# Kernel tuning notes

Hardware: AMD Instinct MI355X
Metric: run time of the kernel (lower is better)

## Reference

```python
import jax, jax.numpy as jnp
import numpy as np

NV = 100000   # vehicle nodes
NE = 100000   # 'edge' nodes (dst type)
E = 250000    # graph edges (connects relation)
VDIM = 16
EDIM = 16
HID = 128
HEADS = 4
DH = 128      # out_feats per head (GATv2Conv(hid, hid))
EPS = 1e-5
NEG_SLOPE = 0.2


def _layernorm(x, g, b):
    mu = x.mean(-1, keepdims=True)
    var = ((x - mu) ** 2).mean(-1, keepdims=True)
    return (x - mu) * jax.lax.rsqrt(var + EPS) * g + b


def setup_inputs() -> dict:
    key = jax.random.key(0)
    ks = jax.random.split(key, 20)
    s = 0.05
    return {
        "v_feat": jax.random.normal(ks[0], (NV, VDIM), jnp.float32),
        "e_feat": jax.random.normal(ks[1], (NE, EDIM), jnp.float32),
        "Wv": jax.random.normal(ks[2], (VDIM, HID), jnp.float32) * s,
        "bv": jnp.zeros((HID,), jnp.float32),
        "gv": jnp.ones((HID,), jnp.float32),
        "betav": jnp.zeros((HID,), jnp.float32),
        "We": jax.random.normal(ks[3], (EDIM, HID), jnp.float32) * s,
        "be": jnp.zeros((HID,), jnp.float32),
        "ge": jnp.ones((HID,), jnp.float32),
        "betae": jnp.zeros((HID,), jnp.float32),
        "Wsrc": jax.random.normal(ks[4], (HID, HEADS * DH), jnp.float32) * s,
        "bsrc": jnp.zeros((HEADS * DH,), jnp.float32),
        "Wdst": jax.random.normal(ks[5], (HID, HEADS * DH), jnp.float32) * s,
        "bdst": jnp.zeros((HEADS * DH,), jnp.float32),
        "attn": jax.random.normal(ks[6], (HEADS, DH), jnp.float32) * s,
        "Wp": jax.random.normal(ks[7], (HID, HID), jnp.float32) * s,
        "bp": jnp.zeros((HID,), jnp.float32),
        "src": jax.random.randint(ks[8], (E,), 0, NV, jnp.int32),
        "dst": jax.random.randint(ks[9], (E,), 0, NE, jnp.int32),
    }


def reference(v_feat, e_feat, Wv, bv, gv, betav, We, be, ge, betae,
              Wsrc, bsrc, Wdst, bdst, attn, Wp, bp, src, dst):
    # --- node-type encoders: Linear -> ReLU -> LayerNorm ---
    h_v = _layernorm(jax.nn.relu(v_feat @ Wv + bv), gv, betav)      # [NV, HID]
    h_e = _layernorm(jax.nn.relu(e_feat @ We + be), ge, betae)      # [NE, HID]

    # --- GATv2Conv (bipartite: vehicle -> edge), 4 heads ---
    fs = (h_v @ Wsrc + bsrc).reshape(NV, HEADS, DH)                 # src proj
    fd = (h_e @ Wdst + bdst).reshape(NE, HEADS, DH)                 # dst proj
    e = jax.nn.leaky_relu(fs[src] + fd[dst], NEG_SLOPE)             # [E, H, D]
    score = jnp.einsum("ehd,hd->eh", e, attn)                       # [E, H]
    # segment-wise (per-dst-node) softmax over incoming edges
    smax = jax.ops.segment_max(score, dst, num_segments=NE)         # [NE, H]
    ex = jnp.exp(score - smax[dst])
    denom = jax.ops.segment_sum(ex, dst, num_segments=NE)
    alpha = ex / denom[dst]                                         # [E, H]
    out = jax.ops.segment_sum(alpha[:, :, None] * fs[src], dst,
                              num_segments=NE)                      # [NE, H, D]

    # HeteroGraphConv mean-aggregate (single relation -> identity),
    # then mean over heads (edge_out.dim()==3 branch)
    edge_out = out.mean(axis=1)                                     # [NE, HID]

    # feature_proj: Linear -> ReLU -> Dropout(eval: identity)
    return jax.nn.relu(edge_out @ Wp + bp)
```

## Files before the change

kernel.cpp:

```cpp
#include <hip/hip_runtime.h>
#include <hip/hip_bf16.h>
#include <math.h>

#define NV 100000
#define NE_N 100000
#define NEDGE 250000
#define NPAD 100032
#define NEG 0.2f
#define LN_EPS 1e-5f

typedef __bf16 bf16_t;
typedef __bf16 bf16x8 __attribute__((ext_vector_type(8)));
typedef float f32x4 __attribute__((ext_vector_type(4)));

__device__ inline unsigned short f2bfu(float f) {
    return __builtin_bit_cast(unsigned short, (__bf16)f);
}
__device__ inline float bfu2f(unsigned short u) {
    return (float)__builtin_bit_cast(__bf16, u);
}
__device__ inline float blo(unsigned w) { return __uint_as_float(w << 16); }
__device__ inline float bhi(unsigned w) { return __uint_as_float(w & 0xffff0000u); }
__device__ inline float lrelu(float x) { return x > 0.f ? x : NEG * x; }
__device__ inline unsigned pk2(float a, float b) {
    return (unsigned)f2bfu(a) | ((unsigned)f2bfu(b) << 16);
}

__device__ __forceinline__ void gload_lds16(const void* g, void* l) {
    __builtin_amdgcn_global_load_lds(
        (const __attribute__((address_space(1))) unsigned int*)g,
        (__attribute__((address_space(3))) unsigned int*)l,
        16, 0, 0);
}

__global__ __launch_bounds__(256) void prep_kernel(
    const float* __restrict__ Wsrc, const float* __restrict__ Wdst,
    const float* __restrict__ Wp, bf16_t* __restrict__ pS,
    bf16_t* __restrict__ pD, bf16_t* __restrict__ pP)
{
    int t = blockIdx.x * 256 + threadIdx.x;
    if (t < 8192) {
        int ksq = t >> 9, col = t & 511;
#pragma unroll
        for (int j = 0; j < 8; ++j)
            pS[(size_t)t * 8 + j] = (bf16_t)Wsrc[(ksq * 8 + j) * 512 + col];
    } else if (t < 16384) {
        int g = t - 8192;
        int ksq = g >> 9, col = g & 511;
#pragma unroll
        for (int j = 0; j < 8; ++j)
            pD[(size_t)g * 8 + j] = (bf16_t)Wdst[(ksq * 8 + j) * 512 + col];
    } else if (t < 18432) {
        int g = t - 16384;
        int ksq = g >> 7, col = g & 127;
#pragma unroll
        for (int j = 0; j < 8; ++j)
            pP[(size_t)g * 8 + j] = (bf16_t)Wp[(ksq * 8 + j) * 128 + col];
    }
}

__global__ __launch_bounds__(256) void count_kernel(
    const int* __restrict__ dst, int* __restrict__ deg)
{
    int t = blockIdx.x * 256 + threadIdx.x;
    if (t < NEDGE) atomicAdd(&deg[dst[t]], 1);
}

__global__ __launch_bounds__(256) void scan1_kernel(
    const int* __restrict__ deg, int* __restrict__ offs, int* __restrict__ bsum)
{
    __shared__ int s[256];
    int i = blockIdx.x * 256 + threadIdx.x;
    int v = (i < NE_N) ? deg[i] : 0;
    s[threadIdx.x] = v;
    __syncthreads();
    for (int off = 1; off < 256; off <<= 1) {
        int t_ = (threadIdx.x >= off) ? s[threadIdx.x - off] : 0;
        __syncthreads();
        s[threadIdx.x] += t_;
        __syncthreads();
    }
    if (i < NE_N) offs[i] = s[threadIdx.x] - v;
    if (threadIdx.x == 255) bsum[blockIdx.x] = s[255];
}

__global__ __launch_bounds__(512) void scan2_kernel(int* __restrict__ bsum, int nb)
{
    __shared__ int s[512];
    int t = threadIdx.x;
    int v = (t < nb) ? bsum[t] : 0;
    s[t] = v;
    __syncthreads();
    for (int off = 1; off < 512; off <<= 1) {
        int t_ = (t >= off) ? s[t - off] : 0;
        __syncthreads();
        s[t] += t_;
        __syncthreads();
    }
    if (t < nb) bsum[t] = s[t] - v;
}

__global__ __launch_bounds__(256) void scan3_kernel(
    int* __restrict__ offs, const int* __restrict__ bsum, int* __restrict__ cursor)
{
    int i = blockIdx.x * 256 + threadIdx.x;
    if (i < NE_N) {
        int o = offs[i] + bsum[blockIdx.x];
        offs[i] = o;
        cursor[i] = o;
    }
}

__global__ __launch_bounds__(256) void scatter_kernel(
    const int* __restrict__ dst, int* __restrict__ cursor, int* __restrict__ eidx)
{
    int t = blockIdx.x * 256 + threadIdx.x;
    if (t < NEDGE) {
        int pos = atomicAdd(&cursor[dst[t]], 1);
        eidx[pos] = t;
    }
}

__global__ __launch_bounds__(256, 4) void enc_proj_kernel(
    const float* __restrict__ featV, const float* __restrict__ WencV,
    const float* __restrict__ bencV, const float* __restrict__ gV,
    const float* __restrict__ betaV, const bf16_t* __restrict__ ApackV,
    const float* __restrict__ bprojV, unsigned short* __restrict__ outV,
    const float* __restrict__ featE, const float* __restrict__ WencE,
    const float* __restrict__ bencE, const float* __restrict__ gE,
    const float* __restrict__ betaE, const bf16_t* __restrict__ ApackE,
    const float* __restrict__ bprojE, unsigned short* __restrict__ outE,
    int nblk1, int M)
{
    __shared__ unsigned short Hs[64 * 136];
    __shared__ __align__(16) unsigned short Abuf[2][8192];
    __shared__ __align__(16) float Bias[512];

    int b = blockIdx.x;
    bool isV = b < nblk1;
    const float* feat  = isV ? featV  : featE;
    const float* Wenc  = isV ? WencV  : WencE;
    const float* benc  = isV ? bencV  : bencE;
    const float* gln   = isV ? gV     : gE;
    const float* beta  = isV ? betaV  : betaE;
    const bf16_t* Apack = isV ? ApackV : ApackE;
    const float* bproj = isV ? bprojV : bprojE;
    unsigned short* out = isV ? outV : outE;
    int row0 = (isV ? b : b - nblk1) * 64;

    int t = threadIdx.x;
    int l = t & 63;
    int w = t >> 6;
    int rbase = __builtin_amdgcn_readfirstlane(w * 16);

    {
        int sr = row0 + rbase + (l >> 2);
        if (sr > M - 1) sr = M - 1;
        gload_lds16(feat + (size_t)sr * 16 + (l & 3) * 4, &Abuf[1][w * 512]);
    }

#pragma unroll
    for (int j = 0; j < 4; ++j) {
        int ksq = w * 4 + j;
        gload_lds16(Apack + ((size_t)(ksq * 512) + l) * 8, &Abuf[0][ksq * 512]);
    }
    if (t < 128)
        *(float4*)&Bias[t * 4] = *(const float4*)(bproj + t * 4);

    float wc0[16], wc1[16];
#pragma unroll
    for (int k = 0; k < 16; ++k) {
        float2 wv = *(const float2*)(Wenc + k * 128 + 2 * l);
        wc0[k] = wv.x;
        wc1[k] = wv.y;
    }
    float2 bv2 = *(const float2*)(benc + 2 * l);

    asm volatile("s_waitcnt vmcnt(0)" ::: "memory");

    const float* Fs = (const float*)&Abuf[1][0];
#pragma unroll
    for (int i = 0; i < 16; ++i) {
        const float* fr = Fs + (rbase + i) * 16;
        float4 f0 = *(const float4*)(fr);
        float4 f1 = *(const float4*)(fr + 4);
        float4 f2 = *(const float4*)(fr + 8);
        float4 f3 = *(const float4*)(fr + 12);
        float a0 = bv2.x, a1 = bv2.y;
        a0 = fmaf(f0.x, wc0[0], a0);  a1 = fmaf(f0.x, wc1[0], a1);
        a0 = fmaf(f0.y, wc0[1], a0);  a1 = fmaf(f0.y, wc1[1], a1);
        a0 = fmaf(f0.z, wc0[2], a0);  a1 = fmaf(f0.z, wc1[2], a1);
        a0 = fmaf(f0.w, wc0[3], a0);  a1 = fmaf(f0.w, wc1[3], a1);
        a0 = fmaf(f1.x, wc0[4], a0);  a1 = fmaf(f1.x, wc1[4], a1);
        a0 = fmaf(f1.y, wc0[5], a0);  a1 = fmaf(f1.y, wc1[5], a1);
        a0 = fmaf(f1.z, wc0[6], a0);  a1 = fmaf(f1.z, wc1[6], a1);
        a0 = fmaf(f1.w, wc0[7], a0);  a1 = fmaf(f1.w, wc1[7], a1);
        a0 = fmaf(f2.x, wc0[8], a0);  a1 = fmaf(f2.x, wc1[8], a1);
        a0 = fmaf(f2.y, wc0[9], a0);  a1 = fmaf(f2.y, wc1[9], a1);
        a0 = fmaf(f2.z, wc0[10], a0); a1 = fmaf(f2.z, wc1[10], a1);
        a0 = fmaf(f2.w, wc0[11], a0); a1 = fmaf(f2.w, wc1[11], a1);
        a0 = fmaf(f3.x, wc0[12], a0); a1 = fmaf(f3.x, wc1[12], a1);
        a0 = fmaf(f3.y, wc0[13], a0); a1 = fmaf(f3.y, wc1[13], a1);
        a0 = fmaf(f3.z, wc0[14], a0); a1 = fmaf(f3.z, wc1[14], a1);
        a0 = fmaf(f3.w, wc0[15], a0); a1 = fmaf(f3.w, wc1[15], a1);
        a0 = fmaxf(a0, 0.f);
        a1 = fmaxf(a1, 0.f);
        *(unsigned*)&Hs[(rbase + i) * 136 + 2 * l] = pk2(a0, a1);
    }

    float s = 0.f, s2 = 0.f;
    {
        int rr = rbase + (l >> 2);
        int q = l & 3;
#pragma unroll
        for (int j = 0; j < 4; ++j) {
            uint4 v = *(const uint4*)&Hs[rr * 136 + q * 32 + j * 8];
            float x;
            x = blo(v.x); s += x; s2 = fmaf(x, x, s2);
            x = bhi(v.x); s += x; s2 = fmaf(x, x, s2);
            x = blo(v.y); s += x; s2 = fmaf(x, x, s2);
            x = bhi(v.y); s += x; s2 = fmaf(x, x, s2);
            x = blo(v.z); s += x; s2 = fmaf(x, x, s2);
            x = bhi(v.z); s += x; s2 = fmaf(x, x, s2);
            x = blo(v.w); s += x; s2 = fmaf(x, x, s2);
            x = bhi(v.w); s += x; s2 = fmaf(x, x, s2);
        }
    }
    s  += __shfl_xor(s, 1, 64);  s  += __shfl_xor(s, 2, 64);
    s2 += __shfl_xor(s2, 1, 64); s2 += __shfl_xor(s2, 2, 64);
    float mu  = s * (1.f / 128.f);
    float var = s2 * (1.f / 128.f) - mu * mu;
    float inv = rsqrtf(var + LN_EPS);

    int kq = l >> 4;
    int ln = l & 15;
    float mu_r  = __shfl(mu,  ln * 4, 64);
    float inv_r = __shfl(inv, ln * 4, 64);

    bf16x8 bfr[4];
#pragma unroll
    for (int ks = 0; ks < 4; ++ks) {
        int c0 = ks * 32 + kq * 8;
        uint4 v = *(const uint4*)&Hs[(rbase + ln) * 136 + c0];
        float4 g0 = *(const float4*)(gln + c0);
        float4 g1 = *(const float4*)(gln + c0 + 4);
        float4 b0 = *(const float4*)(beta + c0);
        float4 b1 = *(const float4*)(beta + c0 + 4);
        uint4 p;
        p.x = pk2(fmaf((blo(v.x) - mu_r) * inv_r, g0.x, b0.x),
                  fmaf((bhi(v.x) - mu_r) * inv_r, g0.y, b0.y));
        p.y = pk2(fmaf((blo(v.y) - mu_r) * inv_r, g0.z, b0.z),
                  fmaf((bhi(v.y) - mu_r) * inv_r, g0.w, b0.w));
        p.z = pk2(fmaf((blo(v.z) - mu_r) * inv_r, g1.x, b1.x),
                  fmaf((bhi(v.z) - mu_r) * inv_r, g1.y, b1.y));
        p.w = pk2(fmaf((blo(v.w) - mu_r) * inv_r, g1.z, b1.z),
                  fmaf((bhi(v.w) - mu_r) * inv_r, g1.w, b1.w));
        bfr[ks] = __builtin_bit_cast(bf16x8, p);
    }

    unsigned short* stag = Hs + rbase * 136;
    int node = row0 + rbase + ln;

#pragma unroll
    for (int p = 0; p < 8; ++p) {
        if (p == 0)
            asm volatile("s_waitcnt lgkmcnt(0)" ::: "memory");
        else
            asm volatile("s_waitcnt vmcnt(2)" ::: "memory");
        __builtin_amdgcn_s_barrier();

        if (p < 7) {
#pragma unroll
            for (int j = 0; j < 4; ++j) {
                int ksq = w * 4 + j;
                gload_lds16(Apack + ((size_t)(ksq * 512 + (p + 1) * 64) + l) * 8,
                            &Abuf[(p + 1) & 1][ksq * 512]);
            }
            __builtin_amdgcn_sched_barrier(0);
        }

        const unsigned short* Ac = Abuf[p & 1];
#pragma unroll
        for (int mt = 0; mt < 4; ++mt) {
            bf16x8 a[4];
#pragma unroll
            for (int ks = 0; ks < 4; ++ks)
                a[ks] = *(const bf16x8*)&Ac[((ks * 4 + kq) * 64 + mt * 16 + ln) * 8];

            f32x4 acc = {0.f, 0.f, 0.f, 0.f};
#pragma unroll
            for (int ks = 0; ks < 4; ++ks)
                acc = __builtin_amdgcn_mfma_f32_16x16x32_bf16(a[ks], bfr[ks], acc, 0, 0, 0);

            int colp = p * 64 + mt * 16 + kq * 4;
            float4 bb = *(const float4*)&Bias[colp];
            ushort4 o;
            o.x = f2bfu(acc[0] + bb.x);
            o.y = f2bfu(acc[1] + bb.y);
            o.z = f2bfu(acc[2] + bb.z);
            o.w = f2bfu(acc[3] + bb.w);
            *(ushort4*)&stag[ln * 136 + mt * 16 + kq * 4] = o;
        }
#pragma unroll
        for (int i = 0; i < 2; ++i) {
            uint4 v = *(const uint4*)&stag[ln * 136 + i * 32 + kq * 8];
            *(uint4*)(out + (size_t)node * 512 + p * 64 + i * 32 + kq * 8) = v;
        }
    }
}

__global__ __launch_bounds__(256) void final_gemm_kernel(
    const float* __restrict__ A, const bf16_t* __restrict__ Ppack,
    const float* __restrict__ bp, float* __restrict__ C, int M)
{
    __shared__ unsigned short Hs[64 * 136];
    int t = threadIdx.x;
    int lane = t & 63;
    int w = t >> 6;
    int row0 = blockIdx.x * 64;

#pragma unroll
    for (int i = 0; i < 8; ++i) {
        int f4 = i * 256 + t;
        int r = f4 >> 5;
        int c4 = (f4 & 31) * 4;
        float4 v = make_float4(0.f, 0.f, 0.f, 0.f);
        if (row0 + r < M)
            v = ((const float4*)(A + (size_t)(row0 + r) * 128))[f4 & 31];
        ushort4 o;
        o.x = f2bfu(v.x); o.y = f2bfu(v.y); o.z = f2bfu(v.z); o.w = f2bfu(v.w);
        *(ushort4*)&Hs[r * 136 + c4] = o;
    }
    __syncthreads();

    int kq = lane >> 4;
    int ln = lane & 15;

    f32x4 acc[2][4];
#pragma unroll
    for (int mt = 0; mt < 2; ++mt)
#pragma unroll
        for (int nt = 0; nt < 4; ++nt) {
            f32x4 z = {0.f, 0.f, 0.f, 0.f};
            acc[mt][nt] = z;
        }

#pragma unroll
    for (int ks = 0; ks < 4; ++ks) {
        bf16x8 bfr[4];
#pragma unroll
        for (int nt = 0; nt < 4; ++nt) {
            const uint4* p = (const uint4*)&Hs[(nt * 16 + ln) * 136 + ks * 32 + kq * 8];
            bfr[nt] = __builtin_bit_cast(bf16x8, *p);
        }
        bf16x8 afr[2];
#pragma unroll
        for (int mt = 0; mt < 2; ++mt) {
            int colA = w * 32 + mt * 16 + ln;
            afr[mt] = *(const bf16x8*)(Ppack + ((size_t)(ks * 4 + kq) * 128 + colA) * 8);
        }
#pragma unroll
        for (int mt = 0; mt < 2; ++mt)
#pragma unroll
            for (int nt = 0; nt < 4; ++nt)
                acc[mt][nt] = __builtin_amdgcn_mfma_f32_16x16x32_bf16(
                    afr[mt], bfr[nt], acc[mt][nt], 0, 0, 0);
    }

#pragma unroll
    for (int mt = 0; mt < 2; ++mt) {
        int col = w * 32 + mt * 16 + kq * 4;
        float4 bb = *(const float4*)(bp + col);
#pragma unroll
        for (int nt = 0; nt < 4; ++nt) {
            int node = row0 + nt * 16 + ln;
            if (node < M) {
                float4 o;
                o.x = fmaxf(acc[mt][nt][0] + bb.x, 0.f);
                o.y = fmaxf(acc[mt][nt][1] + bb.y, 0.f);
                o.z = fmaxf(acc[mt][nt][2] + bb.z, 0.f);
                o.w = fmaxf(acc[mt][nt][3] + bb.w, 0.f);
                *(float4*)(C + (size_t)node * 128 + col) = o;
            }
        }
    }
}

__global__ __launch_bounds__(256) void softagg_kernel(
    const unsigned short* __restrict__ fs, const unsigned short* __restrict__ fdp,
    const float* __restrict__ attn, const int* __restrict__ src,
    const int* __restrict__ offs, const int* __restrict__ deg,
    const int* __restrict__ eidx, float* __restrict__ out)
{
    int d = blockIdx.x * 4 + (threadIdx.x >> 6);
    if (d >= NE_N) return;
    int l = threadIdx.x & 63;
    int r0 = offs[d];
    int n = deg[d];
    int o = l * 8;

    uint4 fv = *(const uint4*)(fdp + (size_t)d * 512 + o);
    float fdv[8] = { blo(fv.x), bhi(fv.x), blo(fv.y), bhi(fv.y),
                     blo(fv.z), bhi(fv.z), blo(fv.w), bhi(fv.w) };
    float4 w0 = *(const float4*)(attn + o);
    float4 w1 = *(const float4*)(attn + o + 4);
    float wv[8] = { w0.x, w0.y, w0.z, w0.w, w1.x, w1.y, w1.z, w1.w };

    float m = -1e30f, sm = 0.f;
    float acc[8];
#pragma unroll
    for (int j = 0; j < 8; ++j) acc[j] = 0.f;

    for (int base = 0; base < n; base += 64) {
        int cnt = min(n - base, 64);
        int sl = 0;
        if (l < cnt) sl = src[eidx[r0 + base + l]];
        for (int i = 0; i < cnt; ++i) {
            int s = __shfl(sl, i, 64);
            uint4 a = *(const uint4*)(fs + (size_t)s * 512 + o);
            float fsv[8] = { blo(a.x), bhi(a.x), blo(a.y), bhi(a.y),
                             blo(a.z), bhi(a.z), blo(a.w), bhi(a.w) };
            float p = 0.f;
#pragma unroll
            for (int j = 0; j < 8; ++j)
                p = fmaf(lrelu(fsv[j] + fdv[j]), wv[j], p);
#pragma unroll
            for (int mk = 1; mk < 16; mk <<= 1)
                p += __shfl_xor(p, mk, 64);
            float mn = fmaxf(m, p);
            float c  = __expf(m - mn);
            float av = __expf(p - mn);
            sm = sm * c + av;
            m = mn;
#pragma unroll
            for (int j = 0; j < 8; ++j)
                acc[j] = fmaf(av, fsv[j], acc[j] * c);
        }
    }

    float inv = (n > 0) ? 0.25f / sm : 0.f;
#pragma unroll
    for (int j = 0; j < 8; ++j) {
        float v = acc[j] * inv;
        v += __shfl_xor(v, 16, 64);
        v += __shfl_xor(v, 32, 64);
        acc[j] = v;
    }
    if (l < 16) {
        float4 o0 = make_float4(acc[0], acc[1], acc[2], acc[3]);
        float4 o1 = make_float4(acc[4], acc[5], acc[6], acc[7]);
        *(float4*)(out + (size_t)d * 128 + l * 8) = o0;
        *(float4*)(out + (size_t)d * 128 + l * 8 + 4) = o1;
    }
}

extern "C" void kernel_launch(void* const* d_in, const int* in_sizes, int n_in,
                              void* d_out, int out_size, void* d_ws, size_t ws_size,
                              hipStream_t stream)
{
    const float* v_feat = (const float*)d_in[0];
    const float* e_feat = (const float*)d_in[1];
    const float* Wv     = (const float*)d_in[2];
    const float* bv     = (const float*)d_in[3];
    const float* gv     = (const float*)d_in[4];
    const float* betav  = (const float*)d_in[5];
    const float* We     = (const float*)d_in[6];
    const float* be     = (const float*)d_in[7];
    const float* ge     = (const float*)d_in[8];
    const float* betae  = (const float*)d_in[9];
    const float* Wsrc   = (const float*)d_in[10];
    const float* bsrc   = (const float*)d_in[11];
    const float* Wdst   = (const float*)d_in[12];
    const float* bdst   = (const float*)d_in[13];
    const float* attn   = (const float*)d_in[14];
    const float* Wp     = (const float*)d_in[15];
    const float* bp     = (const float*)d_in[16];
    const int*   src    = (const int*)d_in[17];
    const int*   dst    = (const int*)d_in[18];
    float* out = (float*)d_out;

    unsigned short* fs = (unsigned short*)d_ws;
    unsigned short* fd = fs + (size_t)NPAD * 512;
    int* deg    = (int*)(fd + (size_t)NPAD * 512);
    int* offs   = deg + NE_N;
    int* cursor = offs + NE_N;
    int* bsum   = cursor + NE_N;
    int* eidx   = bsum + 512;
    bf16_t* pS  = (bf16_t*)(eidx + NEDGE);
    bf16_t* pD  = pS + 65536;
    bf16_t* pP  = pD + 65536;

    const int NB_SCAN = (NE_N + 255) / 256;

    prep_kernel<<<72, 256, 0, stream>>>(Wsrc, Wdst, Wp, pS, pD, pP);

    hipMemsetAsync(deg, 0, (size_t)NE_N * sizeof(int), stream);
    count_kernel<<<(NEDGE + 255) / 256, 256, 0, stream>>>(dst, deg);
    scan1_kernel<<<NB_SCAN, 256, 0, stream>>>(deg, offs, bsum);
    scan2_kernel<<<1, 512, 0, stream>>>(bsum, NB_SCAN);
    scan3_kernel<<<NB_SCAN, 256, 0, stream>>>(offs, bsum, cursor);
    scatter_kernel<<<(NEDGE + 255) / 256, 256, 0, stream>>>(dst, cursor, eidx);

    enc_proj_kernel<<<3126, 256, 0, stream>>>(
        v_feat, Wv, bv, gv, betav, pS, bsrc, fs,
        e_feat, We, be, ge, betae, pD, bdst, fd,
        1563, 100000);

    softagg_kernel<<<NE_N / 4, 256, 0, stream>>>(fs, fd, attn, src, offs, deg,
                                                 eidx, out);

    final_gemm_kernel<<<1563, 256, 0, stream>>>(out, pP, bp, out, NE_N);
}
```

Measured before the change: 297.7 us.

## Fold deg memset into prep, enlarge encoder blocks, pass bf16 intermediate to final GEMM

Zeroes the degree array inside prep_kernel so the separate memset launch is gone. The encoder/projection kernel now uses 512-thread blocks covering 128 rows, which halves the number of blocks and shares each packed-weight load across more rows. Its encoder FMAs are written as packed 2-wide float operations. The aggregation kernel writes its output as bf16 into a workspace buffer, and the final GEMM reads it directly, cutting intermediate traffic and the fp32-to-bf16 conversion. This relies on enough workspace for the extra buffer, the larger LDS footprint per block may reduce occupancy, and NPAD grows to cover the 128-row tiles.

```diff
diff --git a/kernel.cpp b/kernel.cpp
--- a/kernel.cpp
+++ b/kernel.cpp
@@ -5,19 +5,17 @@
 #define NV 100000
 #define NE_N 100000
 #define NEDGE 250000
-#define NPAD 100032
+#define NPAD 100096
 #define NEG 0.2f
 #define LN_EPS 1e-5f
 
 typedef __bf16 bf16_t;
 typedef __bf16 bf16x8 __attribute__((ext_vector_type(8)));
 typedef float f32x4 __attribute__((ext_vector_type(4)));
+typedef float f32x2 __attribute__((ext_vector_type(2)));
 
 __device__ inline unsigned short f2bfu(float f) {
     return __builtin_bit_cast(unsigned short, (__bf16)f);
-}
-__device__ inline float bfu2f(unsigned short u) {
-    return (float)__builtin_bit_cast(__bf16, u);
 }
 __device__ inline float blo(unsigned w) { return __uint_as_float(w << 16); }
 __device__ inline float bhi(unsigned w) { return __uint_as_float(w & 0xffff0000u); }
@@ -36,7 +34,8 @@
 __global__ __launch_bounds__(256) void prep_kernel(
     const float* __restrict__ Wsrc, const float* __restrict__ Wdst,
     const float* __restrict__ Wp, bf16_t* __restrict__ pS,
-    bf16_t* __restrict__ pD, bf16_t* __restrict__ pP)
+    bf16_t* __restrict__ pD, bf16_t* __restrict__ pP,
+    int* __restrict__ deg)
 {
     int t = blockIdx.x * 256 + threadIdx.x;
     if (t < 8192) {
@@ -56,6 +55,9 @@
 #pragma unroll
         for (int j = 0; j < 8; ++j)
             pP[(size_t)g * 8 + j] = (bf16_t)Wp[(ksq * 8 + j) * 128 + col];
+    } else {
+        int z = t - 18432;
+        if (z < NE_N) deg[z] = 0;
     }
 }
 
@@ -121,7 +123,7 @@
     }
 }
 
-__global__ __launch_bounds__(256, 4) void enc_proj_kernel(
+__global__ __launch_bounds__(512, 4) void enc_proj_kernel(
     const float* __restrict__ featV, const float* __restrict__ WencV,
     const float* __restrict__ bencV, const float* __restrict__ gV,
     const float* __restrict__ betaV, const bf16_t* __restrict__ ApackV,
@@ -132,7 +134,7 @@
     const float* __restrict__ bprojE, unsigned short* __restrict__ outE,
     int nblk1, int M)
 {
-    __shared__ unsigned short Hs[64 * 136];
+    __shared__ unsigned short Hs[128 * 136];
     __shared__ __align__(16) unsigned short Abuf[2][8192];
     __shared__ __align__(16) float Bias[512];
 
@@ -146,7 +148,7 @@
     const bf16_t* Apack = isV ? ApackV : ApackE;
     const float* bproj = isV ? bprojV : bprojE;
     unsigned short* out = isV ? outV : outE;
-    int row0 = (isV ? b : b - nblk1) * 64;
+    int row0 = (isV ? b : b - nblk1) * 128;
 
     int t = threadIdx.x;
     int l = t & 63;
@@ -160,19 +162,19 @@
     }
 
 #pragma unroll
-    for (int j = 0; j < 4; ++j) {
-        int ksq = w * 4 + j;
+    for (int j = 0; j < 2; ++j) {
+        int ksq = w * 2 + j;
         gload_lds16(Apack + ((size_t)(ksq * 512) + l) * 8, &Abuf[0][ksq * 512]);
     }
     if (t < 128)
         *(float4*)&Bias[t * 4] = *(const float4*)(bproj + t * 4);
 
-    float wc0[16], wc1[16];
+    f32x2 wc2[16];
 #pragma unroll
     for (int k = 0; k < 16; ++k) {
         float2 wv = *(const float2*)(Wenc + k * 128 + 2 * l);
-        wc0[k] = wv.x;
-        wc1[k] = wv.y;
+        wc2[k][0] = wv.x;
+        wc2[k][1] = wv.y;
     }
     float2 bv2 = *(const float2*)(benc + 2 * l);
 
@@ -186,25 +188,25 @@
         float4 f1 = *(const float4*)(fr + 4);
         float4 f2 = *(const float4*)(fr + 8);
         float4 f3 = *(const float4*)(fr + 12);
-        float a0 = bv2.x, a1 = bv2.y;
-        a0 = fmaf(f0.x, wc0[0], a0);  a1 = fmaf(f0.x, wc1[0], a1);
-        a0 = fmaf(f0.y, wc0[1], a0);  a1 = fmaf(f0.y, wc1[1], a1);
-        a0 = fmaf(f0.z, wc0[2], a0);  a1 = fmaf(f0.z, wc1[2], a1);
-        a0 = fmaf(f0.w, wc0[3], a0);  a1 = fmaf(f0.w, wc1[3], a1);
-        a0 = fmaf(f1.x, wc0[4], a0);  a1 = fmaf(f1.x, wc1[4], a1);
-        a0 = fmaf(f1.y, wc0[5], a0);  a1 = fmaf(f1.y, wc1[5], a1);
-        a0 = fmaf(f1.z, wc0[6], a0);  a1 = fmaf(f1.z, wc1[6], a1);
-        a0 = fmaf(f1.w, wc0[7], a0);  a1 = fmaf(f1.w, wc1[7], a1);
-        a0 = fmaf(f2.x, wc0[8], a0);  a1 = fmaf(f2.x, wc1[8], a1);
-        a0 = fmaf(f2.y, wc0[9], a0);  a1 = fmaf(f2.y, wc1[9], a1);
-        a0 = fmaf(f2.z, wc0[10], a0); a1 = fmaf(f2.z, wc1[10], a1);
-        a0 = fmaf(f2.w, wc0[11], a0); a1 = fmaf(f2.w, wc1[11], a1);
-        a0 = fmaf(f3.x, wc0[12], a0); a1 = fmaf(f3.x, wc1[12], a1);
-        a0 = fmaf(f3.y, wc0[13], a0); a1 = fmaf(f3.y, wc1[13], a1);
-        a0 = fmaf(f3.z, wc0[14], a0); a1 = fmaf(f3.z, wc1[14], a1);
-        a0 = fmaf(f3.w, wc0[15], a0); a1 = fmaf(f3.w, wc1[15], a1);
-        a0 = fmaxf(a0, 0.f);
-        a1 = fmaxf(a1, 0.f);
+        f32x2 a = {bv2.x, bv2.y};
+        a = __builtin_elementwise_fma((f32x2)f0.x, wc2[0],  a);
+        a = __builtin_elementwise_fma((f32x2)f0.y, wc2[1],  a);
+        a = __builtin_elementwise_fma((f32x2)f0.z, wc2[2],  a);
+        a = __builtin_elementwise_fma((f32x2)f0.w, wc2[3],  a);
+        a = __builtin_elementwise_fma((f32x2)f1.x, wc2[4],  a);
+        a = __builtin_elementwise_fma((f32x2)f1.y, wc2[5],  a);
+        a = __builtin_elementwise_fma((f32x2)f1.z, wc2[6],  a);
+        a = __builtin_elementwise_fma((f32x2)f1.w, wc2[7],  a);
+        a = __builtin_elementwise_fma((f32x2)f2.x, wc2[8],  a);
+        a = __builtin_elementwise_fma((f32x2)f2.y, wc2[9],  a);
+        a = __builtin_elementwise_fma((f32x2)f2.z, wc2[10], a);
+        a = __builtin_elementwise_fma((f32x2)f2.w, wc2[11], a);
+        a = __builtin_elementwise_fma((f32x2)f3.x, wc2[12], a);
+        a = __builtin_elementwise_fma((f32x2)f3.y, wc2[13], a);
+        a = __builtin_elementwise_fma((f32x2)f3.z, wc2[14], a);
+        a = __builtin_elementwise_fma((f32x2)f3.w, wc2[15], a);
+        float a0 = fmaxf(a[0], 0.f);
+        float a1 = fmaxf(a[1], 0.f);
         *(unsigned*)&Hs[(rbase + i) * 136 + 2 * l] = pk2(a0, a1);
     }
 
@@ -271,8 +273,8 @@
 
         if (p < 7) {
 #pragma unroll
-            for (int j = 0; j < 4; ++j) {
-                int ksq = w * 4 + j;
+            for (int j = 0; j < 2; ++j) {
+                int ksq = w * 2 + j;
                 gload_lds16(Apack + ((size_t)(ksq * 512 + (p + 1) * 64) + l) * 8,
                             &Abuf[(p + 1) & 1][ksq * 512]);
             }
@@ -310,8 +312,9 @@
 }
 
 __global__ __launch_bounds__(256) void final_gemm_kernel(
-    const float* __restrict__ A, const bf16_t* __restrict__ Ppack,
-    const float* __restrict__ bp, float* __restrict__ C, int M)
+    const float* __restrict__ A, const unsigned short* __restrict__ Abf,
+    const bf16_t* __restrict__ Ppack, const float* __restrict__ bp,
+    float* __restrict__ C, int M)
 {
     __shared__ unsigned short Hs[64 * 136];
     int t = threadIdx.x;
@@ -319,17 +322,30 @@
     int w = t >> 6;
     int row0 = blockIdx.x * 64;
 
-#pragma unroll
-    for (int i = 0; i < 8; ++i) {
-        int f4 = i * 256 + t;
-        int r = f4 >> 5;
-        int c4 = (f4 & 31) * 4;
-        float4 v = make_float4(0.f, 0.f, 0.f, 0.f);
-        if (row0 + r < M)
-            v = ((const float4*)(A + (size_t)(row0 + r) * 128))[f4 & 31];
-        ushort4 o;
-        o.x = f2bfu(v.x); o.y = f2bfu(v.y); o.z = f2bfu(v.z); o.w = f2bfu(v.w);
-        *(ushort4*)&Hs[r * 136 + c4] = o;
+    if (Abf) {
+#pragma unroll
+        for (int i = 0; i < 4; ++i) {
+            int idx = i * 256 + t;
+            int r = idx >> 4;
+            int c = (idx & 15) * 8;
+            uint4 v = make_uint4(0, 0, 0, 0);
+            if (row0 + r < M)
+                v = *(const uint4*)(Abf + (size_t)(row0 + r) * 128 + c);
+            *(uint4*)&Hs[r * 136 + c] = v;
+        }
+    } else {
+#pragma unroll
+        for (int i = 0; i < 8; ++i) {
+            int f4 = i * 256 + t;
+            int r = f4 >> 5;
+            int c4 = (f4 & 31) * 4;
+            float4 v = make_float4(0.f, 0.f, 0.f, 0.f);
+            if (row0 + r < M)
+                v = ((const float4*)(A + (size_t)(row0 + r) * 128))[f4 & 31];
+            ushort4 o;
+            o.x = f2bfu(v.x); o.y = f2bfu(v.y); o.z = f2bfu(v.z); o.w = f2bfu(v.w);
+            *(ushort4*)&Hs[r * 136 + c4] = o;
+        }
     }
     __syncthreads();
 
@@ -390,7 +406,8 @@
     const unsigned short* __restrict__ fs, const unsigned short* __restrict__ fdp,
     const float* __restrict__ attn, const int* __restrict__ src,
     const int* __restrict__ offs, const int* __restrict__ deg,
-    const int* __restrict__ eidx, float* __restrict__ out)
+    const int* __restrict__ eidx, float* __restrict__ outf,
+    unsigned short* __restrict__ eo)
 {
     int d = blockIdx.x * 4 + (threadIdx.x >> 6);
     if (d >= NE_N) return;
@@ -447,10 +464,19 @@
         acc[j] = v;
     }
     if (l < 16) {
-        float4 o0 = make_float4(acc[0], acc[1], acc[2], acc[3]);
-        float4 o1 = make_float4(acc[4], acc[5], acc[6], acc[7]);
-        *(float4*)(out + (size_t)d * 128 + l * 8) = o0;
-        *(float4*)(out + (size_t)d * 128 + l * 8 + 4) = o1;
+        if (eo) {
+            uint4 pk;
+            pk.x = pk2(acc[0], acc[1]);
+            pk.y = pk2(acc[2], acc[3]);
+            pk.z = pk2(acc[4], acc[5]);
+            pk.w = pk2(acc[6], acc[7]);
+            *(uint4*)(eo + (size_t)d * 128 + l * 8) = pk;
+        } else {
+            float4 o0 = make_float4(acc[0], acc[1], acc[2], acc[3]);
+            float4 o1 = make_float4(acc[4], acc[5], acc[6], acc[7]);
+            *(float4*)(outf + (size_t)d * 128 + l * 8) = o0;
+            *(float4*)(outf + (size_t)d * 128 + l * 8 + 4) = o1;
+        }
     }
 }
 
@@ -489,25 +515,28 @@
     bf16_t* pS  = (bf16_t*)(eidx + NEDGE);
     bf16_t* pD  = pS + 65536;
     bf16_t* pP  = pD + 65536;
+    unsigned short* eo = (unsigned short*)(pP + 16384);
+
+    size_t need = (size_t)((char*)(eo + (size_t)NE_N * 128) - (char*)d_ws);
+    if (ws_size < need) eo = nullptr;
 
     const int NB_SCAN = (NE_N + 255) / 256;
 
-    prep_kernel<<<72, 256, 0, stream>>>(Wsrc, Wdst, Wp, pS, pD, pP);
-
-    hipMemsetAsync(deg, 0, (size_t)NE_N * sizeof(int), stream);
+    prep_kernel<<<463, 256, 0, stream>>>(Wsrc, Wdst, Wp, pS, pD, pP, deg);
+
     count_kernel<<<(NEDGE + 255) / 256, 256, 0, stream>>>(dst, deg);
     scan1_kernel<<<NB_SCAN, 256, 0, stream>>>(deg, offs, bsum);
     scan2_kernel<<<1, 512, 0, stream>>>(bsum, NB_SCAN);
     scan3_kernel<<<NB_SCAN, 256, 0, stream>>>(offs, bsum, cursor);
     scatter_kernel<<<(NEDGE + 255) / 256, 256, 0, stream>>>(dst, cursor, eidx);
 
-    enc_proj_kernel<<<3126, 256, 0, stream>>>(
+    enc_proj_kernel<<<1564, 512, 0, stream>>>(
         v_feat, Wv, bv, gv, betav, pS, bsrc, fs,
         e_feat, We, be, ge, betae, pD, bdst, fd,
-        1563, 100000);
+        782, 100000);
 
     softagg_kernel<<<NE_N / 4, 256, 0, stream>>>(fs, fd, attn, src, offs, deg,
-                                                 eidx, out);
-
-    final_gemm_kernel<<<1563, 256, 0, stream>>>(out, pP, bp, out, NE_N);
-}
+                                                 eidx, out, eo);
+
+    final_gemm_kernel<<<1563, 256, 0, stream>>>(out, eo, pP, bp, out, NE_N);
+}
```

New measurement: 291.5 us. 2.1% less time.
